# Kernel tuning notes

Hardware: AMD Instinct MI355X
Metric: run time of the kernel (lower is better)

Reference implementation:

```python
import jax, jax.numpy as jnp
import numpy as np

BS = 4
D = 256
N3 = BS * 80 * 80   # 25600 level-3 nodes
N4 = BS * 40 * 40   # 6400  level-4 nodes
N5 = BS * 20 * 20   # 1600  level-5 nodes
N = N3 + N4 + N5    # 33600 total graph nodes
EC = 260000         # contextual-graph edges (~8-neighborhood lattice)
EH = 120000         # hierarchical-graph edges (cross-scale)


def setup_inputs() -> dict:
    key = jax.random.key(0)
    ks = jax.random.split(key, 16)
    f = lambda k, s: jax.random.normal(k, s, dtype=jnp.float32) * 0.05
    return {
        # backbone features (yolov8-l channel widths)
        'c3': f(ks[0], (BS, 256, 80, 80)),
        'c4': f(ks[1], (BS, 512, 40, 40)),
        'c5': f(ks[2], (BS, 512, 20, 20)),
        # lateral 1x1 convs (stored as [out, in] since kernel is 1x1)
        'w3_1x1': f(ks[3], (256, 256)), 'b3_1x1': jnp.zeros((256,), jnp.float32),
        'w4_1x1': f(ks[4], (256, 512)), 'b4_1x1': jnp.zeros((256,), jnp.float32),
        'w5_1x1': f(ks[5], (256, 512)), 'b5_1x1': jnp.zeros((256,), jnp.float32),
        # output 3x3 convs
        'w3_3x3': f(ks[6], (256, 256, 3, 3)), 'b3_3x3': jnp.zeros((256,), jnp.float32),
        'w4_3x3': f(ks[7], (256, 256, 3, 3)), 'b4_3x3': jnp.zeros((256,), jnp.float32),
        'w5_3x3': f(ks[8], (256, 256, 3, 3)), 'b5_3x3': jnp.zeros((256,), jnp.float32),
        # 6 contextual + 3 hierarchical GNN layers (stacked)
        'Wc': f(ks[9], (6, 256, 256)), 'bc': jnp.zeros((6, 256), jnp.float32),
        'Wh': f(ks[10], (3, 256, 256)), 'bh': jnp.zeros((3, 256), jnp.float32),
        # edge lists (src -> dst message direction)
        'src_c': jax.random.randint(ks[11], (EC,), 0, N, dtype=jnp.int32),
        'dst_c': jax.random.randint(ks[12], (EC,), 0, N, dtype=jnp.int32),
        'src_h': jax.random.randint(ks[13], (EH,), 0, N, dtype=jnp.int32),
        'dst_h': jax.random.randint(ks[14], (EH,), 0, N, dtype=jnp.int32),
    }


def _conv1x1(x, w, b):
    return jnp.einsum('bchw,oc->bohw', x, w) + b[None, :, None, None]


def _conv3x3(x, w, b):
    y = jax.lax.conv_general_dilated(x, w, (1, 1), 'SAME')
    return y + b[None, :, None, None]


def _up2(x):
    return jnp.repeat(jnp.repeat(x, 2, axis=2), 2, axis=3)


def _degree(dst):
    d = jax.ops.segment_sum(jnp.ones(dst.shape, jnp.float32), dst, num_segments=N)
    return jnp.maximum(d, 1.0)[:, None]


def _gnn_layer(h, W, b, src, dst, deg):
    # gather-aggregate-scatter: mean over incoming messages + self, then linear+relu
    agg = jax.ops.segment_sum(h[src], dst, num_segments=N) / deg  # [N, D]
    return jax.nn.relu((h + agg) @ W + b)


def reference(c3, c4, c5,
              w3_1x1, b3_1x1, w4_1x1, b4_1x1, w5_1x1, b5_1x1,
              w3_3x3, b3_3x3, w4_3x3, b4_3x3, w5_3x3, b5_3x3,
              Wc, bc, Wh, bh,
              src_c, dst_c, src_h, dst_h):
    p3 = _conv1x1(c3, w3_1x1, b3_1x1)  # [BS,256,80,80]
    p4 = _conv1x1(c4, w4_1x1, b4_1x1)  # [BS,256,40,40]
    p5 = _conv1x1(c5, w5_1x1, b5_1x1)  # [BS,256,20,20]

    # CNN -> graph node features (NHWC flatten, cat levels)
    h = jnp.concatenate([
        p3.transpose(0, 2, 3, 1).reshape(-1, D),
        p4.transpose(0, 2, 3, 1).reshape(-1, D),
        p5.transpose(0, 2, 3, 1).reshape(-1, D),
    ], axis=0)  # [N, 256]

    deg_c = _degree(dst_c)
    deg_h = _degree(dst_h)
    for i in range(3):                       # context1..3
        h = _gnn_layer(h, Wc[i], bc[i], src_c, dst_c, deg_c)
    for i in range(3):                       # hierarch1..3
        h = _gnn_layer(h, Wh[i], bh[i], src_h, dst_h, deg_h)
    for i in range(3, 6):                    # context4..6
        h = _gnn_layer(h, Wc[i], bc[i], src_c, dst_c, deg_c)

    # graph -> CNN
    p3g = h[:N3].reshape(BS, 80, 80, D).transpose(0, 3, 1, 2)
    p4g = h[N3:N3 + N4].reshape(BS, 40, 40, D).transpose(0, 3, 1, 2)
    p5g = h[N3 + N4:].reshape(BS, 20, 20, D).transpose(0, 3, 1, 2)

    p5 = p5 + p5g
    p4 = p4 + _up2(p5) + p4g
    p3 = p3 + _up2(p4) + p3g

    out3 = _conv3x3(p3, w3_3x3, b3_3x3)
    out4 = _conv3x3(p4, w4_3x3, b4_3x3)
    out5 = _conv3x3(p5, w5_3x3, b5_3x3)
    return out3, out4, out5
```

## Files before the change

kernel.cpp:

```cpp
#include <hip/hip_runtime.h>
#include <stdint.h>

#define N3i 25600
#define N4i 6400
#define N5i 1600
#define NNi 33600
#define ECi 260000
#define EHi 120000

typedef unsigned short u16;
typedef __bf16 bf16x8 __attribute__((ext_vector_type(8)));
typedef float f32x4 __attribute__((ext_vector_type(4)));

__device__ __forceinline__ float b2f(u16 u) {
    union { float f; uint32_t i; } v; v.i = ((uint32_t)u) << 16; return v.f;
}
__device__ __forceinline__ u16 f2b(float f) {
    union { float f; uint32_t i; } v; v.f = f;
    uint32_t x = v.i;
    uint32_t r = (x + 0x7FFFu + ((x >> 16) & 1u)) >> 16;
    return (u16)r;
}

__global__ void detect_kernel(const void* __restrict__ c3raw, int* __restrict__ flag) {
    const uint32_t* p = (const uint32_t*)c3raw;
    int t = threadIdx.x;
    int vote = 0;
    for (int i = t; i < 256; i += 64) {
        uint32_t w = p[i];
        uint32_t lo = w & 0xFFFFu;
        uint32_t e = (lo >> 7) & 0xFFu;
        if (lo == 0u || (e >= 100u && e <= 127u)) vote++;
    }
#pragma unroll
    for (int d = 32; d >= 1; d >>= 1) vote += __shfl_down(vote, d, 64);
    if (t == 0) flag[0] = (vote >= 192) ? 1 : 0;
}

__global__ void zero_i32(int* p, int n) {
    int i = blockIdx.x * 256 + threadIdx.x;
    if (i < n) p[i] = 0;
}

__global__ void hist2_kernel(const int* __restrict__ dst_c, const int* __restrict__ dst_h,
                             int* __restrict__ cnt_c, int* __restrict__ cnt_h) {
    int i = blockIdx.x * 256 + threadIdx.x;
    if (i < ECi) {
        int d = dst_c[i];
        if ((unsigned)d < (unsigned)NNi) atomicAdd(&cnt_c[d], 1);
    } else {
        int j = i - ECi;
        if (j < EHi) {
            int d = dst_h[j];
            if ((unsigned)d < (unsigned)NNi) atomicAdd(&cnt_h[d], 1);
        }
    }
}

__global__ __launch_bounds__(1024) void scan2_kernel(
    const int* __restrict__ cnt_c, int* __restrict__ rs_c, int* __restrict__ cur_c,
    float* __restrict__ inv_c,
    const int* __restrict__ cnt_h, int* __restrict__ rs_h, int* __restrict__ cur_h,
    float* __restrict__ inv_h, int n) {
    const int* cnt = blockIdx.x ? cnt_h : cnt_c;
    int* rs = blockIdx.x ? rs_h : rs_c;
    int* cur = blockIdx.x ? cur_h : cur_c;
    float* inv = blockIdx.x ? inv_h : inv_c;
    __shared__ int ws[16];
    __shared__ int base;
    int t = threadIdx.x, wid = t >> 6, lane = t & 63;
    if (t == 0) { base = 0; rs[0] = 0; }
    __syncthreads();
    for (int i0 = 0; i0 < n; i0 += 1024) {
        int i = i0 + t;
        int v = (i < n) ? cnt[i] : 0;
        int x = v;
#pragma unroll
        for (int d = 1; d < 64; d <<= 1) {
            int y = __shfl_up(x, d, 64);
            if (lane >= d) x += y;
        }
        if (lane == 63) ws[wid] = x;
        __syncthreads();
        if (wid == 0) {
            int s = (lane < 16) ? ws[lane] : 0;
#pragma unroll
            for (int d = 1; d < 16; d <<= 1) {
                int y = __shfl_up(s, d, 64);
                if (lane >= d) s += y;
            }
            if (lane < 16) ws[lane] = s;
        }
        __syncthreads();
        int b = base;
        int incl = x + (wid ? ws[wid - 1] : 0);
        if (i < n) {
            rs[i + 1] = b + incl;
            cur[i] = b + incl - v;
            int dv = v < 1 ? 1 : v;
            inv[i] = 1.0f / (float)dv;
        }
        int tot = ws[15];
        __syncthreads();
        if (t == 1023) base = b + tot;
        __syncthreads();
    }
}

__global__ void fill2_kernel(const int* __restrict__ src_c, const int* __restrict__ dst_c,
                             int* __restrict__ cur_c, int* __restrict__ csr_c,
                             const int* __restrict__ src_h, const int* __restrict__ dst_h,
                             int* __restrict__ cur_h, int* __restrict__ csr_h) {
    int i = blockIdx.x * 256 + threadIdx.x;
    if (i < ECi) {
        int d = dst_c[i];
        if ((unsigned)d < (unsigned)NNi) {
            int p = atomicAdd(&cur_c[d], 1);
            if ((unsigned)p < (unsigned)ECi) csr_c[p] = src_c[i];
        }
    } else {
        int j = i - ECi;
        if (j < EHi) {
            int d = dst_h[j];
            if ((unsigned)d < (unsigned)NNi) {
                int p = atomicAdd(&cur_h[d], 1);
                if ((unsigned)p < (unsigned)EHi) csr_h[p] = src_h[j];
            }
        }
    }
}

struct CvtJobs { const void* src[11]; u16* dst[11]; int n[11]; };

__global__ void cvt_all_kernel(CvtJobs j, const int* __restrict__ flag) {
    int job = blockIdx.y;
    int i = blockIdx.x * 256 + threadIdx.x;
    if (i >= j.n[job]) return;
    const void* s = j.src[job];
    j.dst[job][i] = flag[0] ? ((const u16*)s)[i] : f2b(((const float*)s)[i]);
}

__device__ __forceinline__ void tin_body(const void* in, size_t ioff, u16* outp, int R, int C,
                                         int isb, int c0, int r0, u16 (*tile)[33]) {
    const u16* inb = (const u16*)in + ioff;
    const float* inf_ = (const float*)in + ioff;
    int tx = threadIdx.x, ty = threadIdx.y;
#pragma unroll
    for (int i = 0; i < 4; i++) {
        int r = r0 + ty + i * 8, c = c0 + tx;
        if (r < R && c < C) {
            size_t idx = (size_t)r * C + c;
            tile[ty + i * 8][tx] = isb ? inb[idx] : f2b(inf_[idx]);
        }
    }
    __syncthreads();
#pragma unroll
    for (int i = 0; i < 4; i++) {
        int c = c0 + ty + i * 8, r = r0 + tx;
        if (c < C && r < R) outp[(size_t)c * R + r] = tile[tx][ty + i * 8];
    }
}

__global__ void transpose_in3(const void* __restrict__ c3, const void* __restrict__ c4,
                              const void* __restrict__ c5, u16* __restrict__ Xt3,
                              u16* __restrict__ Xt4, u16* __restrict__ Xt5,
                              const int* __restrict__ flag) {
    __shared__ u16 tile[32][33];
    int bx = blockIdx.x;
    const void* in; u16* outb; int R, C, xb;
    if (bx < 200)      { in = c3; outb = Xt3; R = 256; C = 6400; xb = bx; }
    else if (bx < 250) { in = c4; outb = Xt4; R = 512; C = 1600; xb = bx - 200; }
    else               { in = c5; outb = Xt5; R = 512; C = 400;  xb = bx - 250; }
    int r0 = blockIdx.y * 32;
    if (r0 >= R) return;
    size_t boff = (size_t)blockIdx.z * R * C;
    tin_body(in, boff, outb + boff, R, C, flag[0], xb * 32, r0, tile);
}

__global__ void transpose_w(const void* __restrict__ Wc, const void* __restrict__ Wh,
                            u16* __restrict__ WtG, const int* __restrict__ flag) {
    __shared__ u16 tile[32][33];
    int z = blockIdx.z;
    const void* in = (z < 6) ? Wc : Wh;
    int zi = (z < 6) ? z : z - 6;
    tin_body(in, (size_t)zi * 65536, WtG + (size_t)z * 65536, 256, 256, flag[0],
             blockIdx.x * 32, blockIdx.y * 32, tile);
}

__global__ void transpose_out3(const u16* __restrict__ OutT, void* __restrict__ outv,
                               const int* __restrict__ flag) {
    __shared__ u16 tile[32][33];
    int by = blockIdx.y;
    const u16* inb; size_t out_off; int R, yb;
    if (by < 200)      { inb = OutT; out_off = 0; R = 6400; yb = by; }
    else if (by < 250) { inb = OutT + (size_t)N3i * 256; out_off = (size_t)4 * 256 * 6400; R = 1600; yb = by - 200; }
    else               { inb = OutT + (size_t)(N3i + N4i) * 256; out_off = (size_t)4 * 256 * 8000; R = 400; yb = by - 250; }
    int r0 = yb * 32;
    if (r0 >= R) return;
    const int C = 256;
    int isb = flag[0];
    int c0 = blockIdx.x * 32;
    size_t boff = (size_t)blockIdx.z * R * C;
    const u16* inp = inb + boff;
    int tx = threadIdx.x, ty = threadIdx.y;
#pragma unroll
    for (int i = 0; i < 4; i++) {
        int r = r0 + ty + i * 8, c = c0 + tx;
        if (r < R && c < C) tile[ty + i * 8][tx] = inp[(size_t)r * C + c];
    }
    __syncthreads();
#pragma unroll
    for (int i = 0; i < 4; i++) {
        int c = c0 + ty + i * 8, r = r0 + tx;
        if (c < C && r < R) {
            size_t o = out_off + boff + (size_t)c * R + r;
            u16 v = tile[tx][ty + i * 8];
            if (isb) ((u16*)outv)[o] = v;
            else ((float*)outv)[o] = b2f(v);
        }
    }
}

__global__ void convw3_kernel(const void* __restrict__ w0, const void* __restrict__ w1,
                              const void* __restrict__ w2, u16* __restrict__ WtC,
                              const int* __restrict__ flag) {
    int lvl = blockIdx.y;
    const void* w = (lvl == 0) ? w0 : (lvl == 1) ? w1 : w2;
    u16* wt = WtC + (size_t)lvl * 256 * 2304;
    int i = blockIdx.x * 256 + threadIdx.x;
    if (i >= 256 * 2304) return;
    int n = i / 2304;
    int k = i - n * 2304;
    int tap = k >> 8, ci = k & 255;
    int si = n * 2304 + ci * 9 + tap;
    wt[i] = flag[0] ? ((const u16*)w)[si] : f2b(((const float*)w)[si]);
}

__global__ __launch_bounds__(256) void gather_kernel(
    const u16* __restrict__ H, const int* __restrict__ csr, const int* __restrict__ rs,
    const float* __restrict__ invdeg, u16* __restrict__ T, int ecap) {
    int node = blockIdx.x * 4 + (threadIdx.x >> 6);
    if (node >= NNi) return;
    int lane = threadIdx.x & 63;
    int c = lane * 4;
    int e0 = rs[node], e1 = rs[node + 1];
    e0 = e0 < 0 ? 0 : e0;
    e1 = e1 > ecap ? ecap : e1;
    float s0 = 0.f, s1 = 0.f, s2 = 0.f, s3 = 0.f;
    int srcn = (e0 < e1) ? csr[e0] : 0;
    for (int e = e0; e < e1; e++) {
        int src = srcn;
        if (e + 1 < e1) srcn = csr[e + 1];
        src = ((unsigned)src < (unsigned)NNi) ? src : 0;
        ushort4 hv = *(const ushort4*)(H + (size_t)src * 256 + c);
        s0 += b2f(hv.x); s1 += b2f(hv.y); s2 += b2f(hv.z); s3 += b2f(hv.w);
    }
    float inv = invdeg[node];
    ushort4 hv = *(const ushort4*)(H + (size_t)node * 256 + c);
    ushort4 o;
    o.x = f2b(b2f(hv.x) + s0 * inv);
    o.y = f2b(b2f(hv.y) + s1 * inv);
    o.z = f2b(b2f(hv.z) + s2 * inv);
    o.w = f2b(b2f(hv.w) + s3 * inv);
    *(ushort4*)(T + (size_t)node * 256 + c) = o;
}

template <bool CONV, bool RELU>
__device__ __forceinline__ void gemm_body(
    u16 (* __restrict__ As)[40], u16 (* __restrict__ Bs)[40],
    const u16* __restrict__ A, int lda,
    const u16* __restrict__ Bt, int ldb,
    const u16* __restrict__ bias,
    u16* __restrict__ out, u16* __restrict__ out2,
    int M, int K, int H, int W, int m0, int n0) {
    int t = threadIdx.x;
    int wave = t >> 6, lane = t & 63;
    int wm = wave & 1, wn = wave >> 1;
    f32x4 acc[4][4] = {};

    int r = t >> 1;
    int seg = (t & 1) * 16;

    int arow = m0 + r;
    bool arow_ok = arow < M;
    int y_ = 0, x_ = 0;
    if (CONV && arow_ok) {
        int HW = H * W;
        int b = arow / HW;
        int rem = arow - b * HW;
        y_ = rem / W;
        x_ = rem - y_ * W;
    }
    const u16* aptr = A + (size_t)arow * lda + seg;
    const u16* bptr = Bt + (size_t)(n0 + r) * ldb + seg;

    uint4 av0, av1, bv0, bv1;
    auto load_a = [&](int k0) {
        uint4 z = make_uint4(0, 0, 0, 0);
        av0 = z; av1 = z;
        if (!CONV) {
            if (arow_ok) {
                av0 = *(const uint4*)(aptr + k0);
                av1 = *(const uint4*)(aptr + k0 + 8);
            }
        } else {
            int tap = k0 >> 8;
            int ty = tap / 3;
            int dy = ty - 1, dx = tap - ty * 3 - 1;
            int yy = y_ + dy, xx = x_ + dx;
            if (arow_ok && (unsigned)yy < (unsigned)H && (unsigned)xx < (unsigned)W) {
                const u16* p = A + (size_t)(arow + dy * W + dx) * lda + (k0 & 255) + seg;
                av0 = *(const uint4*)p;
                av1 = *(const uint4*)(p + 8);
            }
        }
    };

    load_a(0);
    bv0 = *(const uint4*)(bptr);
    bv1 = *(const uint4*)(bptr + 8);

    for (int k0 = 0; k0 < K; k0 += 32) {
        __syncthreads();
        *(uint4*)&As[r][seg] = av0;
        *(uint4*)&As[r][seg + 8] = av1;
        *(uint4*)&Bs[r][seg] = bv0;
        *(uint4*)&Bs[r][seg + 8] = bv1;
        __syncthreads();
        int kn = k0 + 32;
        if (kn < K) {
            load_a(kn);
            bv0 = *(const uint4*)(bptr + kn);
            bv1 = *(const uint4*)(bptr + kn + 8);
        }
        int fm = lane & 15;
        int kq = (lane >> 4) * 8;
        bf16x8 af[4], bfv[4];
#pragma unroll
        for (int i = 0; i < 4; i++) af[i] = *(const bf16x8*)&As[wm * 64 + i * 16 + fm][kq];
#pragma unroll
        for (int j = 0; j < 4; j++) bfv[j] = *(const bf16x8*)&Bs[wn * 64 + j * 16 + fm][kq];
#pragma unroll
        for (int i = 0; i < 4; i++)
#pragma unroll
            for (int j = 0; j < 4; j++)
                acc[i][j] = __builtin_amdgcn_mfma_f32_16x16x32_bf16(af[i], bfv[j], acc[i][j], 0, 0, 0);
    }

    int q = lane >> 4, nl = lane & 15;
#pragma unroll
    for (int j = 0; j < 4; j++) {
        int n = n0 + wn * 64 + j * 16 + nl;
        float bv = b2f(bias[n]);
#pragma unroll
        for (int i = 0; i < 4; i++) {
            int mbase = m0 + wm * 64 + i * 16 + q * 4;
#pragma unroll
            for (int rg = 0; rg < 4; rg++) {
                int m = mbase + rg;
                if (m < M) {
                    float v = acc[i][j][rg] + bv;
                    if (RELU) v = fmaxf(v, 0.f);
                    u16 bs = f2b(v);
                    out[(size_t)m * 256 + n] = bs;
                    if (out2) out2[(size_t)m * 256 + n] = bs;
                }
            }
        }
    }
}

template <bool CONV, bool RELU>
__global__ __launch_bounds__(256) void gemm_kernel(
    const u16* __restrict__ A, int lda,
    const u16* __restrict__ Bt, int ldb,
    const u16* __restrict__ bias,
    u16* __restrict__ out, u16* __restrict__ out2,
    int M, int K, int H, int W) {
    __shared__ __align__(16) u16 As[128][40];
    __shared__ __align__(16) u16 Bs[128][40];
    gemm_body<CONV, RELU>(As, Bs, A, lda, Bt, ldb, bias, out, out2, M, K, H, W,
                          blockIdx.y * 128, blockIdx.x * 128);
}

__global__ __launch_bounds__(256) void lat_all_kernel(
    const u16* __restrict__ Xt3, const u16* __restrict__ Xt4, const u16* __restrict__ Xt5,
    const u16* __restrict__ W1, const u16* __restrict__ BB,
    u16* __restrict__ P, u16* __restrict__ Ha) {
    __shared__ __align__(16) u16 As[128][40];
    __shared__ __align__(16) u16 Bs[128][40];
    int by = blockIdx.y;
    const u16* A; const u16* Bt; const u16* bias;
    int K, Ml, m0; size_t off;
    if (by < 200)      { A = Xt3; Bt = W1;          bias = BB;       K = 256; Ml = N3i; off = 0;                          m0 = by * 128; }
    else if (by < 250) { A = Xt4; Bt = W1 + 65536;  bias = BB + 256; K = 512; Ml = N4i; off = (size_t)N3i * 256;          m0 = (by - 200) * 128; }
    else               { A = Xt5; Bt = W1 + 196608; bias = BB + 512; K = 512; Ml = N5i; off = (size_t)(N3i + N4i) * 256;  m0 = (by - 250) * 128; }
    gemm_body<false, false>(As, Bs, A, K, Bt, K, bias, P + off, Ha + off, Ml, K, 0, 0,
                            m0, blockIdx.x * 128);
}

__global__ __launch_bounds__(256) void conv_gemm_all(
    const u16* __restrict__ Pc, const u16* __restrict__ WtC,
    const u16* __restrict__ BB, u16* __restrict__ OutT) {
    __shared__ __align__(16) u16 As[128][40];
    __shared__ __align__(16) u16 Bs[128][40];
    int by = blockIdx.y;
    int lvl, yl, Hd, Ml; size_t base;
    if (by < 200)      { lvl = 0; yl = by;       Hd = 80; Ml = N3i; base = 0; }
    else if (by < 250) { lvl = 1; yl = by - 200; Hd = 40; Ml = N4i; base = (size_t)N3i * 256; }
    else               { lvl = 2; yl = by - 250; Hd = 20; Ml = N5i; base = (size_t)(N3i + N4i) * 256; }
    gemm_body<true, false>(As, Bs, Pc + base, 256, WtC + (size_t)lvl * 256 * 2304, 2304,
                           BB + 3072 + lvl * 256, OutT + base, nullptr,
                           Ml, 2304, Hd, Hd, yl * 128, blockIdx.x * 128);
}

__global__ void pyr_kernel(const u16* __restrict__ P, const u16* __restrict__ Hf,
                           u16* __restrict__ Pc) {
    int i = blockIdx.x * 256 + threadIdx.x;
    if (i >= NNi * 64) return;
    int node = i >> 6, c = (i & 63) * 4;
    size_t bi = (size_t)node * 256 + c;
    ushort4 pv = *(const ushort4*)(P + bi);
    ushort4 hv = *(const ushort4*)(Hf + bi);
    float v0 = b2f(pv.x) + b2f(hv.x);
    float v1 = b2f(pv.y) + b2f(hv.y);
    float v2 = b2f(pv.z) + b2f(hv.z);
    float v3 = b2f(pv.w) + b2f(hv.w);
    if (node < N3i) {
        int b = node / 6400, rem = node - b * 6400;
        int y = rem / 80, x = rem - y * 80;
        size_t s4 = ((size_t)N3i + b * 1600 + (y >> 1) * 40 + (x >> 1)) * 256 + c;
        size_t s5 = ((size_t)(N3i + N4i) + b * 400 + (y >> 2) * 20 + (x >> 2)) * 256 + c;
        ushort4 p4 = *(const ushort4*)(P + s4), h4 = *(const ushort4*)(Hf + s4);
        ushort4 p5 = *(const ushort4*)(P + s5), h5 = *(const ushort4*)(Hf + s5);
        v0 += b2f(p4.x) + b2f(h4.x) + b2f(p5.x) + b2f(h5.x);
        v1 += b2f(p4.y) + b2f(h4.y) + b2f(p5.y) + b2f(h5.y);
        v2 += b2f(p4.z) + b2f(h4.z) + b2f(p5.z) + b2f(h5.z);
        v3 += b2f(p4.w) + b2f(h4.w) + b2f(p5.w) + b2f(h5.w);
    } else if (node < N3i + N4i) {
        int n4 = node - N3i;
        int b = n4 / 1600, rem = n4 - b * 1600;
        int y = rem / 40, x = rem - y * 40;
        size_t s5 = ((size_t)(N3i + N4i) + b * 400 + (y >> 1) * 20 + (x >> 1)) * 256 + c;
        ushort4 p5 = *(const ushort4*)(P + s5), h5 = *(const ushort4*)(Hf + s5);
        v0 += b2f(p5.x) + b2f(h5.x);
        v1 += b2f(p5.y) + b2f(h5.y);
        v2 += b2f(p5.z) + b2f(h5.z);
        v3 += b2f(p5.w) + b2f(h5.w);
    }
    ushort4 o;
    o.x = f2b(v0); o.y = f2b(v1); o.z = f2b(v2); o.w = f2b(v3);
    *(ushort4*)(Pc + bi) = o;
}

extern "C" void kernel_launch(void* const* d_in, const int* in_sizes, int n_in,
                              void* d_out, int out_size, void* d_ws, size_t ws_size,
                              hipStream_t stream) {
    (void)in_sizes; (void)n_in; (void)out_size; (void)ws_size;
    const void* c3 = d_in[0];
    const void* c4 = d_in[1];
    const void* c5 = d_in[2];
    const void* w3_1 = d_in[3];
    const void* b3_1 = d_in[4];
    const void* w4_1 = d_in[5];
    const void* b4_1 = d_in[6];
    const void* w5_1 = d_in[7];
    const void* b5_1 = d_in[8];
    const void* w3_3 = d_in[9];
    const void* b3_3 = d_in[10];
    const void* w4_3 = d_in[11];
    const void* b4_3 = d_in[12];
    const void* w5_3 = d_in[13];
    const void* b5_3 = d_in[14];
    const void* Wc = d_in[15];
    const void* bc = d_in[16];
    const void* Wh = d_in[17];
    const void* bh = d_in[18];
    const int* src_c = (const int*)d_in[19];
    const int* dst_c = (const int*)d_in[20];
    const int* src_h = (const int*)d_in[21];
    const int* dst_h = (const int*)d_in[22];

    char* w = (char*)d_ws;
    auto alloc = [&](size_t bytes) -> void* {
        void* p = (void*)w;
        w += (bytes + 255) & ~(size_t)255;
        return p;
    };
    u16* XT  = (u16*)alloc(((size_t)N3i * 256 + (size_t)N4i * 512 + (size_t)N5i * 512) * 2);
    u16* Xt3 = XT;
    u16* Xt4 = XT + (size_t)N3i * 256;
    u16* Xt5 = Xt4 + (size_t)N4i * 512;
    u16* T   = XT;
    u16* Pc  = XT;
    u16* WtC = XT + (size_t)NNi * 256;
    u16* WtG = (u16*)alloc((size_t)9 * 65536 * 2);
    u16* W1  = (u16*)alloc((size_t)(65536 + 131072 + 131072) * 2);
    u16* BB  = (u16*)alloc((size_t)3840 * 2);
    u16* P   = (u16*)alloc((size_t)NNi * 256 * 2);
    u16* Ha  = (u16*)alloc((size_t)NNi * 256 * 2);
    u16* Hb  = (u16*)d_out;
    int* csr_c = (int*)alloc((size_t)ECi * 4);
    int* csr_h = (int*)alloc((size_t)EHi * 4);
    int* cnt2  = (int*)alloc((size_t)2 * NNi * 4);
    int* cnt_c = cnt2;
    int* cnt_h = cnt2 + NNi;
    int* rs_c  = (int*)alloc((size_t)(NNi + 1) * 4);
    int* rs_h  = (int*)alloc((size_t)(NNi + 1) * 4);
    int* cur_c = (int*)alloc((size_t)NNi * 4);
    int* cur_h = (int*)alloc((size_t)NNi * 4);
    float* inv_c = (float*)alloc((size_t)NNi * 4);
    float* inv_h = (float*)alloc((size_t)NNi * 4);
    int* flag  = (int*)alloc(256);

    detect_kernel<<<1, 64, 0, stream>>>(c3, flag);

    zero_i32<<<(2 * NNi + 255) / 256, 256, 0, stream>>>(cnt2, 2 * NNi);
    hist2_kernel<<<(ECi + EHi + 255) / 256, 256, 0, stream>>>(dst_c, dst_h, cnt_c, cnt_h);
    scan2_kernel<<<2, 1024, 0, stream>>>(cnt_c, rs_c, cur_c, inv_c,
                                         cnt_h, rs_h, cur_h, inv_h, NNi);
    fill2_kernel<<<(ECi + EHi + 255) / 256, 256, 0, stream>>>(
        src_c, dst_c, cur_c, csr_c, src_h, dst_h, cur_h, csr_h);

    CvtJobs cj;
    cj.src[0] = w3_1; cj.dst[0] = W1;          cj.n[0] = 65536;
    cj.src[1] = w4_1; cj.dst[1] = W1 + 65536;  cj.n[1] = 131072;
    cj.src[2] = w5_1; cj.dst[2] = W1 + 196608; cj.n[2] = 131072;
    cj.src[3] = b3_1; cj.dst[3] = BB;          cj.n[3] = 256;
    cj.src[4] = b4_1; cj.dst[4] = BB + 256;    cj.n[4] = 256;
    cj.src[5] = b5_1; cj.dst[5] = BB + 512;    cj.n[5] = 256;
    cj.src[6] = bc;   cj.dst[6] = BB + 768;    cj.n[6] = 1536;
    cj.src[7] = bh;   cj.dst[7] = BB + 2304;   cj.n[7] = 768;
    cj.src[8] = b3_3; cj.dst[8] = BB + 3072;   cj.n[8] = 256;
    cj.src[9] = b4_3; cj.dst[9] = BB + 3328;   cj.n[9] = 256;
    cj.src[10] = b5_3; cj.dst[10] = BB + 3584; cj.n[10] = 256;
    cvt_all_kernel<<<dim3(512, 11), 256, 0, stream>>>(cj, flag);

    transpose_in3<<<dim3(263, 16, 4), dim3(32, 8), 0, stream>>>(c3, c4, c5, Xt3, Xt4, Xt5, flag);
    transpose_w<<<dim3(8, 8, 9), dim3(32, 8), 0, stream>>>(Wc, Wh, WtG, flag);

    lat_all_kernel<<<dim3(2, 263), 256, 0, stream>>>(Xt3, Xt4, Xt5, W1, BB, P, Ha);

    convw3_kernel<<<dim3(2304, 3), 256, 0, stream>>>(w3_3, w4_3, w5_3, WtC, flag);

    u16* Hcur = Ha;
    u16* Hnxt = Hb;
    for (int l = 0; l < 9; l++) {
        bool ctx = (l < 3) || (l >= 6);
        const int* csr = ctx ? csr_c : csr_h;
        const int* rs = ctx ? rs_c : rs_h;
        const float* inv = ctx ? inv_c : inv_h;
        int ecap = ctx ? ECi : EHi;
        int wi = (l < 3) ? l : (l < 6 ? 6 + (l - 3) : l - 3);
        const u16* bias = (l < 3) ? BB + 768 + l * 256
                        : (l < 6 ? BB + 2304 + (l - 3) * 256 : BB + 768 + (l - 3) * 256);
        gather_kernel<<<(NNi + 3) / 4, 256, 0, stream>>>(Hcur, csr, rs, inv, T, ecap);
        gemm_kernel<false, true><<<dim3(2, 263), 256, 0, stream>>>(
            T, 256, WtG + (size_t)wi * 65536, 256, bias, Hnxt, nullptr, NNi, 256, 0, 0);
        u16* tmp = Hcur; Hcur = Hnxt; Hnxt = tmp;
    }
    u16* OutT = Hnxt;

    pyr_kernel<<<(NNi * 64 + 255) / 256, 256, 0, stream>>>(P, Hcur, Pc);

    conv_gemm_all<<<dim3(2, 263), 256, 0, stream>>>(Pc, WtC, BB, OutT);

    transpose_out3<<<dim3(8, 263, 4), dim3(32, 8), 0, stream>>>(OutT, d_out, flag);
}
```

Baseline: 735.9 us.

## Use direct global-to-LDS loads with double-buffered swizzled tiles; widen gather to 8 channels

The shared GEMM body now copies A/B tiles straight into LDS with global_load_lds, using two buffers and an XOR swizzle. This replaces the register-staged copy and its double barrier, so the next tile's loads overlap the current tile's MFMAs. Out-of-range and padded rows point at a small zeroed buffer instead of using predicated register zeroing. The gather kernel splits each node's edges across two half-waves with 8-channel vector loads and combines them with a cross-half shuffle. Risks: per-lane LDS address mapping for global_load_lds, and idle lanes in the gather on low-degree nodes.

```diff
diff --git a/kernel.cpp b/kernel.cpp
--- a/kernel.cpp
+++ b/kernel.cpp
@@ -11,6 +11,7 @@
 typedef unsigned short u16;
 typedef __bf16 bf16x8 __attribute__((ext_vector_type(8)));
 typedef float f32x4 __attribute__((ext_vector_type(4)));
+typedef unsigned short u16x8 __attribute__((ext_vector_type(8)));
 
 __device__ __forceinline__ float b2f(u16 u) {
     union { float f; uint32_t i; } v; v.i = ((uint32_t)u) << 16; return v.f;
@@ -22,9 +23,16 @@
     return (u16)r;
 }
 
-__global__ void detect_kernel(const void* __restrict__ c3raw, int* __restrict__ flag) {
+__device__ __forceinline__ void gll16(const u16* g, u16* l) {
+    __builtin_amdgcn_global_load_lds((const __attribute__((address_space(1))) void*)g,
+                                     (__attribute__((address_space(3))) void*)l, 16, 0, 0);
+}
+
+__global__ void detect_kernel(const void* __restrict__ c3raw, int* __restrict__ flag,
+                              uint32_t* __restrict__ zp) {
     const uint32_t* p = (const uint32_t*)c3raw;
     int t = threadIdx.x;
+    zp[t] = 0;
     int vote = 0;
     for (int i = t; i < 256; i += 64) {
         uint32_t w = p[i];
@@ -242,109 +250,121 @@
     int node = blockIdx.x * 4 + (threadIdx.x >> 6);
     if (node >= NNi) return;
     int lane = threadIdx.x & 63;
-    int c = lane * 4;
+    int half = lane >> 5;
+    int c = (lane & 31) * 8;
     int e0 = rs[node], e1 = rs[node + 1];
     e0 = e0 < 0 ? 0 : e0;
     e1 = e1 > ecap ? ecap : e1;
-    float s0 = 0.f, s1 = 0.f, s2 = 0.f, s3 = 0.f;
-    int srcn = (e0 < e1) ? csr[e0] : 0;
-    for (int e = e0; e < e1; e++) {
+    const u16* Hn = H + (size_t)node * 256 + c;
+    u16x8 self = *(const u16x8*)Hn;
+    float s0 = 0.f, s1 = 0.f, s2 = 0.f, s3 = 0.f, s4 = 0.f, s5 = 0.f, s6 = 0.f, s7 = 0.f;
+    int e = e0 + half;
+    int srcn = (e < e1) ? csr[e] : 0;
+    for (; e < e1; e += 2) {
         int src = srcn;
-        if (e + 1 < e1) srcn = csr[e + 1];
+        if (e + 2 < e1) srcn = csr[e + 2];
         src = ((unsigned)src < (unsigned)NNi) ? src : 0;
-        ushort4 hv = *(const ushort4*)(H + (size_t)src * 256 + c);
-        s0 += b2f(hv.x); s1 += b2f(hv.y); s2 += b2f(hv.z); s3 += b2f(hv.w);
-    }
-    float inv = invdeg[node];
-    ushort4 hv = *(const ushort4*)(H + (size_t)node * 256 + c);
-    ushort4 o;
-    o.x = f2b(b2f(hv.x) + s0 * inv);
-    o.y = f2b(b2f(hv.y) + s1 * inv);
-    o.z = f2b(b2f(hv.z) + s2 * inv);
-    o.w = f2b(b2f(hv.w) + s3 * inv);
-    *(ushort4*)(T + (size_t)node * 256 + c) = o;
+        u16x8 hv = *(const u16x8*)(H + (size_t)src * 256 + c);
+        s0 += b2f(hv[0]); s1 += b2f(hv[1]); s2 += b2f(hv[2]); s3 += b2f(hv[3]);
+        s4 += b2f(hv[4]); s5 += b2f(hv[5]); s6 += b2f(hv[6]); s7 += b2f(hv[7]);
+    }
+    s0 += __shfl_xor(s0, 32, 64); s1 += __shfl_xor(s1, 32, 64);
+    s2 += __shfl_xor(s2, 32, 64); s3 += __shfl_xor(s3, 32, 64);
+    s4 += __shfl_xor(s4, 32, 64); s5 += __shfl_xor(s5, 32, 64);
+    s6 += __shfl_xor(s6, 32, 64); s7 += __shfl_xor(s7, 32, 64);
+    if (half == 0) {
+        float inv = invdeg[node];
+        u16x8 o;
+        o[0] = f2b(b2f(self[0]) + s0 * inv); o[1] = f2b(b2f(self[1]) + s1 * inv);
+        o[2] = f2b(b2f(self[2]) + s2 * inv); o[3] = f2b(b2f(self[3]) + s3 * inv);
+        o[4] = f2b(b2f(self[4]) + s4 * inv); o[5] = f2b(b2f(self[5]) + s5 * inv);
+        o[6] = f2b(b2f(self[6]) + s6 * inv); o[7] = f2b(b2f(self[7]) + s7 * inv);
+        *(u16x8*)(T + (size_t)node * 256 + c) = o;
+    }
 }
 
 template <bool CONV, bool RELU>
 __device__ __forceinline__ void gemm_body(
-    u16 (* __restrict__ As)[40], u16 (* __restrict__ Bs)[40],
+    u16 (* __restrict__ lds)[4096],
     const u16* __restrict__ A, int lda,
     const u16* __restrict__ Bt, int ldb,
     const u16* __restrict__ bias,
+    const u16* __restrict__ zp,
     u16* __restrict__ out, u16* __restrict__ out2,
     int M, int K, int H, int W, int m0, int n0) {
     int t = threadIdx.x;
-    int wave = t >> 6, lane = t & 63;
-    int wm = wave & 1, wn = wave >> 1;
+    int w = t >> 6, lane = t & 63;
+    int wm = w & 1, wn = w >> 1;
     f32x4 acc[4][4] = {};
 
-    int r = t >> 1;
-    int seg = (t & 1) * 16;
-
-    int arow = m0 + r;
-    bool arow_ok = arow < M;
-    int y_ = 0, x_ = 0;
-    if (CONV && arow_ok) {
+    int g0 = w * 128 + lane;
+    int g1 = g0 + 64;
+    int row0 = g0 >> 2, c0 = g0 & 3;
+    int row1 = g1 >> 2, c1 = g1 & 3;
+    int ss0 = ((c0 ^ ((row0 >> 1) & 3)) << 3);
+    int ss1 = ((c1 ^ ((row1 >> 1) & 3)) << 3);
+
+    int ar0 = m0 + row0, ar1 = m0 + row1;
+    bool aok0 = ar0 < M, aok1 = ar1 < M;
+    int y0_ = 0, x0_ = 0, y1_ = 0, x1_ = 0;
+    if (CONV) {
         int HW = H * W;
-        int b = arow / HW;
-        int rem = arow - b * HW;
-        y_ = rem / W;
-        x_ = rem - y_ * W;
-    }
-    const u16* aptr = A + (size_t)arow * lda + seg;
-    const u16* bptr = Bt + (size_t)(n0 + r) * ldb + seg;
-
-    uint4 av0, av1, bv0, bv1;
-    auto load_a = [&](int k0) {
-        uint4 z = make_uint4(0, 0, 0, 0);
-        av0 = z; av1 = z;
+        if (aok0) { int b = ar0 / HW; int rem = ar0 - b * HW; y0_ = rem / W; x0_ = rem - y0_ * W; }
+        if (aok1) { int b = ar1 / HW; int rem = ar1 - b * HW; y1_ = rem / W; x1_ = rem - y1_ * W; }
+    }
+    const u16* aP0 = A + (size_t)ar0 * lda + ss0;
+    const u16* aP1 = A + (size_t)ar1 * lda + ss1;
+    const u16* bP0 = Bt + (size_t)(n0 + row0) * ldb + ss0;
+    const u16* bP1 = Bt + (size_t)(n0 + row1) * ldb + ss1;
+
+    int lbase = w * 1024;
+
+    auto stage = [&](int bf, int k0) {
+        u16* LA = lds[bf * 2];
+        u16* LB = lds[bf * 2 + 1];
+        const u16* sa0;
+        const u16* sa1;
         if (!CONV) {
-            if (arow_ok) {
-                av0 = *(const uint4*)(aptr + k0);
-                av1 = *(const uint4*)(aptr + k0 + 8);
-            }
+            sa0 = aok0 ? aP0 + k0 : zp;
+            sa1 = aok1 ? aP1 + k0 : zp;
         } else {
             int tap = k0 >> 8;
-            int ty = tap / 3;
-            int dy = ty - 1, dx = tap - ty * 3 - 1;
-            int yy = y_ + dy, xx = x_ + dx;
-            if (arow_ok && (unsigned)yy < (unsigned)H && (unsigned)xx < (unsigned)W) {
-                const u16* p = A + (size_t)(arow + dy * W + dx) * lda + (k0 & 255) + seg;
-                av0 = *(const uint4*)p;
-                av1 = *(const uint4*)(p + 8);
-            }
-        }
+            int t3 = tap / 3;
+            int dy = t3 - 1, dx = tap - t3 * 3 - 1;
+            int off = (dy * W + dx) * lda + (k0 & 255);
+            int yy0 = y0_ + dy, xx0 = x0_ + dx;
+            int yy1 = y1_ + dy, xx1 = x1_ + dx;
+            sa0 = (aok0 && (unsigned)yy0 < (unsigned)H && (unsigned)xx0 < (unsigned)W) ? aP0 + off : zp;
+            sa1 = (aok1 && (unsigned)yy1 < (unsigned)H && (unsigned)xx1 < (unsigned)W) ? aP1 + off : zp;
+        }
+        gll16(sa0, LA + lbase);
+        gll16(sa1, LA + lbase + 512);
+        gll16(bP0 + k0, LB + lbase);
+        gll16(bP1 + k0, LB + lbase + 512);
     };
 
-    load_a(0);
-    bv0 = *(const uint4*)(bptr);
-    bv1 = *(const uint4*)(bptr + 8);
-
-    for (int k0 = 0; k0 < K; k0 += 32) {
-        __syncthreads();
-        *(uint4*)&As[r][seg] = av0;
-        *(uint4*)&As[r][seg + 8] = av1;
-        *(uint4*)&Bs[r][seg] = bv0;
-        *(uint4*)&Bs[r][seg + 8] = bv1;
-        __syncthreads();
-        int kn = k0 + 32;
-        if (kn < K) {
-            load_a(kn);
-            bv0 = *(const uint4*)(bptr + kn);
-            bv1 = *(const uint4*)(bptr + kn + 8);
-        }
-        int fm = lane & 15;
-        int kq = (lane >> 4) * 8;
+    int nst = K >> 5;
+    int fm = lane & 15;
+    int co = (((lane >> 4) ^ ((fm >> 1) & 3)) << 3);
+
+    stage(0, 0);
+    __syncthreads();
+    for (int s = 0; s < nst; s++) {
+        int bf = s & 1;
+        if (s + 1 < nst) stage(bf ^ 1, (s + 1) << 5);
+        const u16* LA = lds[bf * 2];
+        const u16* LB = lds[bf * 2 + 1];
         bf16x8 af[4], bfv[4];
 #pragma unroll
-        for (int i = 0; i < 4; i++) af[i] = *(const bf16x8*)&As[wm * 64 + i * 16 + fm][kq];
-#pragma unroll
-        for (int j = 0; j < 4; j++) bfv[j] = *(const bf16x8*)&Bs[wn * 64 + j * 16 + fm][kq];
+        for (int i = 0; i < 4; i++) af[i] = *(const bf16x8*)&LA[(wm * 64 + i * 16 + fm) * 32 + co];
+#pragma unroll
+        for (int j = 0; j < 4; j++) bfv[j] = *(const bf16x8*)&LB[(wn * 64 + j * 16 + fm) * 32 + co];
 #pragma unroll
         for (int i = 0; i < 4; i++)
 #pragma unroll
             for (int j = 0; j < 4; j++)
                 acc[i][j] = __builtin_amdgcn_mfma_f32_16x16x32_bf16(af[i], bfv[j], acc[i][j], 0, 0, 0);
+        __syncthreads();
     }
 
     int q = lane >> 4, nl = lane & 15;
@@ -375,42 +395,40 @@
     const u16* __restrict__ A, int lda,
     const u16* __restrict__ Bt, int ldb,
     const u16* __restrict__ bias,
+    const u16* __restrict__ zp,
     u16* __restrict__ out, u16* __restrict__ out2,
     int M, int K, int H, int W) {
-    __shared__ __align__(16) u16 As[128][40];
-    __shared__ __align__(16) u16 Bs[128][40];
-    gemm_body<CONV, RELU>(As, Bs, A, lda, Bt, ldb, bias, out, out2, M, K, H, W,
+    __shared__ __align__(16) u16 lds[4][4096];
+    gemm_body<CONV, RELU>(lds, A, lda, Bt, ldb, bias, zp, out, out2, M, K, H, W,
                           blockIdx.y * 128, blockIdx.x * 128);
 }
 
 __global__ __launch_bounds__(256) void lat_all_kernel(
     const u16* __restrict__ Xt3, const u16* __restrict__ Xt4, const u16* __restrict__ Xt5,
-    const u16* __restrict__ W1, const u16* __restrict__ BB,
+    const u16* __restrict__ W1, const u16* __restrict__ BB, const u16* __restrict__ zp,
     u16* __restrict__ P, u16* __restrict__ Ha) {
-    __shared__ __align__(16) u16 As[128][40];
-    __shared__ __align__(16) u16 Bs[128][40];
+    __shared__ __align__(16) u16 lds[4][4096];
     int by = blockIdx.y;
     const u16* A; const u16* Bt; const u16* bias;
     int K, Ml, m0; size_t off;
     if (by < 200)      { A = Xt3; Bt = W1;          bias = BB;       K = 256; Ml = N3i; off = 0;                          m0 = by * 128; }
     else if (by < 250) { A = Xt4; Bt = W1 + 65536;  bias = BB + 256; K = 512; Ml = N4i; off = (size_t)N3i * 256;          m0 = (by - 200) * 128; }
     else               { A = Xt5; Bt = W1 + 196608; bias = BB + 512; K = 512; Ml = N5i; off = (size_t)(N3i + N4i) * 256;  m0 = (by - 250) * 128; }
-    gemm_body<false, false>(As, Bs, A, K, Bt, K, bias, P + off, Ha + off, Ml, K, 0, 0,
+    gemm_body<false, false>(lds, A, K, Bt, K, bias, zp, P + off, Ha + off, Ml, K, 0, 0,
                             m0, blockIdx.x * 128);
 }
 
 __global__ __launch_bounds__(256) void conv_gemm_all(
     const u16* __restrict__ Pc, const u16* __restrict__ WtC,
-    const u16* __restrict__ BB, u16* __restrict__ OutT) {
-    __shared__ __align__(16) u16 As[128][40];
-    __shared__ __align__(16) u16 Bs[128][40];
+    const u16* __restrict__ BB, const u16* __restrict__ zp, u16* __restrict__ OutT) {
+    __shared__ __align__(16) u16 lds[4][4096];
     int by = blockIdx.y;
     int lvl, yl, Hd, Ml; size_t base;
     if (by < 200)      { lvl = 0; yl = by;       Hd = 80; Ml = N3i; base = 0; }
     else if (by < 250) { lvl = 1; yl = by - 200; Hd = 40; Ml = N4i; base = (size_t)N3i * 256; }
     else               { lvl = 2; yl = by - 250; Hd = 20; Ml = N5i; base = (size_t)(N3i + N4i) * 256; }
-    gemm_body<true, false>(As, Bs, Pc + base, 256, WtC + (size_t)lvl * 256 * 2304, 2304,
-                           BB + 3072 + lvl * 256, OutT + base, nullptr,
+    gemm_body<true, false>(lds, Pc + base, 256, WtC + (size_t)lvl * 256 * 2304, 2304,
+                           BB + 3072 + lvl * 256, zp, OutT + base, nullptr,
                            Ml, 2304, Hd, Hd, yl * 128, blockIdx.x * 128);
 }
 
@@ -512,8 +530,9 @@
     float* inv_c = (float*)alloc((size_t)NNi * 4);
     float* inv_h = (float*)alloc((size_t)NNi * 4);
     int* flag  = (int*)alloc(256);
-
-    detect_kernel<<<1, 64, 0, stream>>>(c3, flag);
+    u16* zp    = (u16*)alloc(256);
+
+    detect_kernel<<<1, 64, 0, stream>>>(c3, flag, (uint32_t*)zp);
 
     zero_i32<<<(2 * NNi + 255) / 256, 256, 0, stream>>>(cnt2, 2 * NNi);
     hist2_kernel<<<(ECi + EHi + 255) / 256, 256, 0, stream>>>(dst_c, dst_h, cnt_c, cnt_h);
@@ -539,7 +558,7 @@
     transpose_in3<<<dim3(263, 16, 4), dim3(32, 8), 0, stream>>>(c3, c4, c5, Xt3, Xt4, Xt5, flag);
     transpose_w<<<dim3(8, 8, 9), dim3(32, 8), 0, stream>>>(Wc, Wh, WtG, flag);
 
-    lat_all_kernel<<<dim3(2, 263), 256, 0, stream>>>(Xt3, Xt4, Xt5, W1, BB, P, Ha);
+    lat_all_kernel<<<dim3(2, 263), 256, 0, stream>>>(Xt3, Xt4, Xt5, W1, BB, zp, P, Ha);
 
     convw3_kernel<<<dim3(2304, 3), 256, 0, stream>>>(w3_3, w4_3, w5_3, WtC, flag);
 
@@ -556,14 +575,14 @@
                         : (l < 6 ? BB + 2304 + (l - 3) * 256 : BB + 768 + (l - 3) * 256);
         gather_kernel<<<(NNi + 3) / 4, 256, 0, stream>>>(Hcur, csr, rs, inv, T, ecap);
         gemm_kernel<false, true><<<dim3(2, 263), 256, 0, stream>>>(
-            T, 256, WtG + (size_t)wi * 65536, 256, bias, Hnxt, nullptr, NNi, 256, 0, 0);
+            T, 256, WtG + (size_t)wi * 65536, 256, bias, zp, Hnxt, nullptr, NNi, 256, 0, 0);
         u16* tmp = Hcur; Hcur = Hnxt; Hnxt = tmp;
     }
     u16* OutT = Hnxt;
 
     pyr_kernel<<<(NNi * 64 + 255) / 256, 256, 0, stream>>>(P, Hcur, Pc);
 
-    conv_gemm_all<<<dim3(2, 263), 256, 0, stream>>>(Pc, WtC, BB, OutT);
+    conv_gemm_all<<<dim3(2, 263), 256, 0, stream>>>(Pc, WtC, BB, zp, OutT);
 
     transpose_out3<<<dim3(8, 263, 4), dim3(32, 8), 0, stream>>>(OutT, d_out, flag);
 }
```

Result: faster. 686.7 us (-6.7%).
